# Kernel optimization log

Hardware: AMD Instinct MI355X
Metric: run time of the kernel (lower is better)

## Reference

```python
import jax, jax.numpy as jnp
import numpy as np

EPS = 1e-5
GROUPS = 32


def setup_inputs() -> dict:
    key = jax.random.key(0)
    ks = jax.random.split(key, 12)
    b, c, h, w = 8, 256, 64, 64
    s = 1.0 / np.sqrt(c)
    return {
        "x": jax.random.normal(ks[0], (b, c, h, w), jnp.float32),
        "gn_w": jax.random.uniform(ks[1], (c,), jnp.float32, 0.5, 1.5),
        "gn_b": jax.random.normal(ks[2], (c,), jnp.float32) * 0.1,
        "wq": jax.random.normal(ks[3], (c, c), jnp.float32) * s,
        "bq": jax.random.normal(ks[4], (c,), jnp.float32) * 0.02,
        "wk": jax.random.normal(ks[5], (c, c), jnp.float32) * s,
        "bk": jax.random.normal(ks[6], (c,), jnp.float32) * 0.02,
        "wv": jax.random.normal(ks[7], (c, c), jnp.float32) * s,
        "bv": jax.random.normal(ks[8], (c,), jnp.float32) * 0.02,
        "wp": jax.random.normal(ks[9], (c, c), jnp.float32) * s,
        "bp": jax.random.normal(ks[10], (c,), jnp.float32) * 0.02,
        "gamma": jax.random.normal(ks[11], (1,), jnp.float32),
    }


def _group_norm(x, weight, bias):
    b, c, h, w = x.shape
    g = min(c, GROUPS)
    xg = x.reshape(b, g, c // g, h * w)
    mean = xg.mean(axis=(2, 3), keepdims=True)
    var = jnp.var(xg, axis=(2, 3), keepdims=True)
    xn = (xg - mean) * jax.lax.rsqrt(var + EPS)
    xn = xn.reshape(b, c, h, w)
    return xn * weight[None, :, None, None] + bias[None, :, None, None]


def reference(x, gn_w, gn_b, wq, bq, wk, bk, wv, bv, wp, bp, gamma):
    b, c, h, w = x.shape
    x_dash = _group_norm(x, gn_w, gn_b)           # (b,c,h,w)
    xf = x_dash.reshape(b, c, h * w)              # (b,c,n)
    # 1x1 convs == per-pixel linear maps over channels
    q = jnp.einsum('oc,bcn->bon', wq, xf) + bq[None, :, None]
    k = jnp.einsum('oc,bcn->bon', wk, xf) + bk[None, :, None]
    v = jnp.einsum('oc,bcn->bon', wv, xf) + bv[None, :, None]
    # attn[b,i,j] = <q[:,i], k[:,j]> / sqrt(c)
    attn = jnp.einsum('bci,bcj->bij', q, k) / jnp.sqrt(jnp.asarray(c, x.dtype))
    attn = jax.nn.softmax(attn, axis=-1)
    # out[b,c,i] = sum_j v[b,c,j] * attn[b,i,j]
    out = jnp.einsum('bcj,bij->bci', v, attn)
    out = jnp.einsum('oc,bcn->bon', wp, out) + bp[None, :, None]
    out = out.reshape(b, c, h, w)
    return x + gamma[0] * out
```

## Files before the change

kernel.cpp:

```cpp
#include <hip/hip_runtime.h>
#include <cstdint>
#include <cstddef>


#define NB   8
#define NC   256
#define NPIX 4096
#define CPG  8

typedef __attribute__((ext_vector_type(8))) short bf16x8;
typedef __attribute__((ext_vector_type(4))) short s16x4;
typedef __attribute__((ext_vector_type(8))) short s16x8;
typedef __attribute__((ext_vector_type(4))) float f32x4;

__device__ __forceinline__ short f2bf(float f) {
  union { float f; uint32_t u; } v; v.f = f;
  return (short)((v.u + 0x7fffu + ((v.u >> 16) & 1u)) >> 16);
}

__device__ __forceinline__ uint32_t cvtpk_bf(float a, float b) {
  uint32_t r;
  asm("v_cvt_pk_bf16_f32 %0, %1, %2" : "=v"(r) : "v"(a), "v"(b));
  return r;
}

__device__ __forceinline__ f32x4 mfma16(bf16x8 a, bf16x8 b, f32x4 c) {
  return __builtin_amdgcn_mfma_f32_16x16x32_bf16(a, b, c, 0, 0, 0);
}

__device__ __forceinline__ void gload_lds16(const short* g, short* l) {
  __builtin_amdgcn_global_load_lds(
      (const __attribute__((address_space(1))) void*)g,
      (__attribute__((address_space(3))) void*)l, 16, 0, 0);
}

__global__ __launch_bounds__(256) void wconv4(
    const float* __restrict__ w0, const float* __restrict__ w1,
    const float* __restrict__ w2, const float* __restrict__ w3,
    short* __restrict__ o0, short* __restrict__ o1,
    short* __restrict__ o2, short* __restrict__ o3) {
  int m = blockIdx.x >> 6;
  const float* w = (m == 0) ? w0 : (m == 1) ? w1 : (m == 2) ? w2 : w3;
  short* o = (m == 0) ? o0 : (m == 1) ? o1 : (m == 2) ? o2 : o3;
  int i = ((blockIdx.x & 63) * 256 + threadIdx.x) * 4;
  float4 v = *reinterpret_cast<const float4*>(w + i);
  s16x4 p;
  p[0] = f2bf(v.x); p[1] = f2bf(v.y); p[2] = f2bf(v.z); p[3] = f2bf(v.w);
  *reinterpret_cast<s16x4*>(o + i) = p;
}

__global__ __launch_bounds__(1024) void gnorm(const float* __restrict__ x,
                                              const float* __restrict__ gw,
                                              const float* __restrict__ gb,
                                              short* __restrict__ xdt) {
  int b = blockIdx.x >> 5;
  int g = blockIdx.x & 31;
  const float* xp = x + ((size_t)b * NC + (size_t)g * CPG) * NPIX;
  int t = threadIdx.x;

  float s = 0.f, ss = 0.f;
  const float4* xp4 = reinterpret_cast<const float4*>(xp);
  for (int i = t; i < (CPG * NPIX) / 4; i += 1024) {
    float4 v = xp4[i];
    s  += v.x + v.y + v.z + v.w;
    ss += v.x * v.x + v.y * v.y + v.z * v.z + v.w * v.w;
  }
  for (int m = 32; m; m >>= 1) { s += __shfl_xor(s, m); ss += __shfl_xor(ss, m); }
  __shared__ float red[34];
  int wid = t >> 6;
  if ((t & 63) == 0) { red[wid] = s; red[16 + wid] = ss; }
  __syncthreads();
  if (t == 0) {
    float a = 0.f, b2 = 0.f;
    for (int i = 0; i < 16; ++i) { a += red[i]; b2 += red[16 + i]; }
    float mean = a * (1.f / 32768.f);
    float var  = b2 * (1.f / 32768.f) - mean * mean;
    red[32] = mean;
    red[33] = rsqrtf(var + 1e-5f);
  }
  __syncthreads();
  float mean = red[32], rstd = red[33];

  float wv2[CPG], bv2[CPG];
  for (int cc = 0; cc < CPG; ++cc) {
    float wgt = gw[g * CPG + cc] * rstd;
    wv2[cc] = wgt;
    bv2[cc] = gb[g * CPG + cc] - mean * wgt;
  }
  for (int pix = t; pix < NPIX; pix += 1024) {
    s16x8 pk;
    for (int cc = 0; cc < CPG; ++cc)
      pk[cc] = f2bf(fmaf(xp[cc * NPIX + pix], wv2[cc], bv2[cc]));
    *reinterpret_cast<s16x8*>(&xdt[((size_t)b * NPIX + pix) * NC + g * CPG]) = pk;
  }
}

__global__ __launch_bounds__(256) void qkv_gemm(
    const short* __restrict__ wq_bf, const short* __restrict__ wk_bf,
    const short* __restrict__ wv_bf,
    const float* __restrict__ bq, const float* __restrict__ bk,
    const float* __restrict__ bv,
    const short* __restrict__ xdt,
    short* __restrict__ qt, short* __restrict__ kt, short* __restrict__ vv) {
  int nt = blockIdx.x, b = blockIdx.y;

  __shared__ short xtile[64 * 256];
  __shared__ float bias_lds[3][256];
  int t = threadIdx.x;
  const short* xg = xdt + ((size_t)b * NPIX + nt * 64) * NC;
  for (int it = 0; it < 8; ++it) {
    int id = t + it * 256, row = id >> 5, part = id & 31;
    *reinterpret_cast<uint4*>(&xtile[row * 256 + (part ^ (row & 7)) * 8]) =
        *reinterpret_cast<const uint4*>(&xg[(size_t)row * 256 + part * 8]);
  }
  bias_lds[0][t] = bq[t];
  bias_lds[1][t] = bk[t];
  bias_lds[2][t] = bv[t];
  __syncthreads();

  int w = t >> 6, lane = t & 63, g = lane >> 4, lr = lane & 15;
  const short* Ws[3] = {wq_bf, wk_bf, wv_bf};

  for (int mi = 0; mi < 3; ++mi) {
    const short* W = Ws[mi];
    f32x4 acc[4][4];
    f32x4 zz = {0.f, 0.f, 0.f, 0.f};
    for (int i = 0; i < 4; ++i) for (int j = 0; j < 4; ++j) acc[i][j] = zz;

    for (int c0 = 0; c0 < 256; c0 += 32) {
      bf16x8 af[4], bfr[4];
      for (int mf = 0; mf < 4; ++mf)
        af[mf] = *reinterpret_cast<const bf16x8*>(
            &W[(size_t)(w * 64 + mf * 16 + lr) * 256 + c0 + g * 8]);
      for (int nf = 0; nf < 4; ++nf) {
        int row = nf * 16 + lr;
        bfr[nf] = *reinterpret_cast<const bf16x8*>(
            &xtile[row * 256 + (((c0 >> 3) + g) ^ (row & 7)) * 8]);
      }
      for (int mf = 0; mf < 4; ++mf)
        for (int nf = 0; nf < 4; ++nf)
          acc[mf][nf] = mfma16(af[mf], bfr[nf], acc[mf][nf]);
    }

    if (mi < 2) {
      short* outp = (mi == 0) ? qt : kt;
      for (int mf = 0; mf < 4; ++mf)
        for (int nf = 0; nf < 4; ++nf) {
          int ob = w * 64 + mf * 16 + g * 4;
          int n  = nt * 64 + nf * 16 + lr;
          s16x4 pk;
          for (int r = 0; r < 4; ++r)
            pk[r] = f2bf(acc[mf][nf][r] + bias_lds[mi][ob + r]);
          *reinterpret_cast<s16x4*>(&outp[((size_t)b * NPIX + n) * NC + ob]) = pk;
        }
    } else {
      for (int mf = 0; mf < 4; ++mf)
        for (int nf = 0; nf < 4; ++nf) {
          int ob = w * 64 + mf * 16 + g * 4;
          int n  = nt * 64 + nf * 16 + lr;
          for (int r = 0; r < 4; ++r)
            vv[((size_t)b * NC + ob + r) * NPIX + n] =
                f2bf(acc[mf][nf][r] + bias_lds[2][ob + r]);
        }
    }
  }
}

__global__ __launch_bounds__(256, 2) void attn(
    const short* __restrict__ qt, const short* __restrict__ kt,
    const short* __restrict__ vv, short* __restrict__ ot) {
  int b = blockIdx.x, itile = blockIdx.y;
  __shared__ short ktile[64 * 256];
  __shared__ short Pb[2][64 * 64];
  __shared__ float alpha_lds[2][64];
  __shared__ float exch[2][64];

  int t = threadIdx.x, w = t >> 6, lane = t & 63, g = lane >> 4, lr = lane & 15;
  int kk = w >> 1, qq = w & 1;
  int i0 = itile * 64;

  const short* ktg = kt + (size_t)b * NPIX * NC;

  for (int it = 0; it < 8; ++it) {
    int id = it * 256 + t, row = id >> 5, ch = id & 31;
    gload_lds16(ktg + row * 256 + (ch ^ (row & 7)) * 8, &ktile[id * 8]);
  }
  const short* kgp = ktg + 16384;

  bf16x8 qf[2][8];
  for (int qi = 0; qi < 2; ++qi) {
    const short* qrow =
        qt + ((size_t)b * NPIX + i0 + 32 * qq + 16 * qi + lr) * NC;
    for (int ks = 0; ks < 8; ++ks)
      qf[qi][ks] = *reinterpret_cast<const bf16x8*>(&qrow[ks * 32 + g * 8]);
  }

  const short* vbase =
      vv + (size_t)b * NC * NPIX + (size_t)(w * 64 + lr) * NPIX + g * 8;

  int row0 = 32 * kk + lr, row1 = row0 + 16;
  int eidx[2], pwo[2][2];
  for (int qi = 0; qi < 2; ++qi) {
    int q_loc = 32 * qq + 16 * qi + lr;
    eidx[qi] = q_loc;
    for (int mt = 0; mt < 2; ++mt)
      pwo[qi][mt] = q_loc * 64 +
                    (((4 * kk + 2 * mt + (g >> 1)) ^ (q_loc & 7)) * 8) +
                    (g & 1) * 4;
  }
  int pr[4][2];
  for (int nf = 0; nf < 4; ++nf)
    for (int ks2 = 0; ks2 < 2; ++ks2) {
      int qc = nf * 16 + lr;
      pr[nf][ks2] = qc * 64 + (((ks2 * 4 + g) ^ (qc & 7)) * 8);
    }

  f32x4 zz = {0.f, 0.f, 0.f, 0.f};
  f32x4 oacc[4][4];
  for (int i = 0; i < 4; ++i) for (int j = 0; j < 4; ++j) oacc[i][j] = zz;
  bf16x8 va0[4], va1[4];
  float m_[2] = {-1e30f, -1e30f}, l_p[2] = {0.f, 0.f};

  const float sc = 0.0625f, L2E = 1.44269504f;
  const float SCL = sc * L2E;

  for (int jt = 0; jt < 64; ++jt) {
    int cur = jt & 1, prv = cur ^ 1;

    asm volatile("s_waitcnt vmcnt(0) lgkmcnt(0)" ::: "memory");
    __builtin_amdgcn_s_barrier();
    asm volatile("" ::: "memory");

    if (jt > 0) {
      float av[4];
#pragma unroll
      for (int nf = 0; nf < 4; ++nf) av[nf] = alpha_lds[prv][nf * 16 + lr];
      if (__any((av[0] != 1.f) | (av[1] != 1.f) | (av[2] != 1.f) | (av[3] != 1.f))) {
#pragma unroll
        for (int mf = 0; mf < 4; ++mf)
#pragma unroll
          for (int nf = 0; nf < 4; ++nf) oacc[mf][nf] *= av[nf];
      }
      __builtin_amdgcn_s_setprio(1);
      bf16x8 pb[4];
#pragma unroll
      for (int nf = 0; nf < 4; ++nf)
        pb[nf] = *reinterpret_cast<const bf16x8*>(&Pb[prv][pr[nf][0]]);
#pragma unroll
      for (int mf = 0; mf < 4; ++mf)
#pragma unroll
        for (int nf = 0; nf < 4; ++nf)
          oacc[mf][nf] = mfma16(va0[mf], pb[nf], oacc[mf][nf]);
      __builtin_amdgcn_s_setprio(0);
      const short* vp = vbase + (size_t)(jt - 1) * 64 + 32;
#pragma unroll
      for (int mf = 0; mf < 4; ++mf)
        va1[mf] = *reinterpret_cast<const bf16x8*>(vp + (size_t)mf * (16 * NPIX));
    }

    f32x4 s[2][2];
    s[0][0] = zz; s[0][1] = zz; s[1][0] = zz; s[1][1] = zz;
    __builtin_amdgcn_s_setprio(1);
#pragma unroll
    for (int ks = 0; ks < 8; ++ks) {
      bf16x8 kf0 = *reinterpret_cast<const bf16x8*>(
          &ktile[row0 * 256 + (((ks * 4) + g) ^ (row0 & 7)) * 8]);
      bf16x8 kf1 = *reinterpret_cast<const bf16x8*>(
          &ktile[row1 * 256 + (((ks * 4) + g) ^ (row1 & 7)) * 8]);
      s[0][0] = mfma16(kf0, qf[0][ks], s[0][0]);
      s[0][1] = mfma16(kf0, qf[1][ks], s[0][1]);
      s[1][0] = mfma16(kf1, qf[0][ks], s[1][0]);
      s[1][1] = mfma16(kf1, qf[1][ks], s[1][1]);
    }
    __builtin_amdgcn_s_setprio(0);

    float mx[2];
#pragma unroll
    for (int qi = 0; qi < 2; ++qi) {
      float m0 = fmaxf(fmaxf(s[0][qi][0], s[0][qi][1]),
                       fmaxf(s[0][qi][2], s[0][qi][3]));
      float m1 = fmaxf(fmaxf(s[1][qi][0], s[1][qi][1]),
                       fmaxf(s[1][qi][2], s[1][qi][3]));
      float m = fmaxf(m0, m1);
      m = fmaxf(m, __shfl_xor(m, 16));
      m = fmaxf(m, __shfl_xor(m, 32));
      mx[qi] = m;
    }
    if (lane < 16) {
      exch[kk][32 * qq + lr]      = mx[0];
      exch[kk][32 * qq + 16 + lr] = mx[1];
    }

    asm volatile("s_waitcnt lgkmcnt(0)" ::: "memory");
    __builtin_amdgcn_s_barrier();
    asm volatile("" ::: "memory");

    for (int it = 0; it < 8; ++it) {
      int id = it * 256 + t, row = id >> 5, ch = id & 31;
      gload_lds16(kgp + row * 256 + (ch ^ (row & 7)) * 8, &ktile[id * 8]);
    }
    kgp += 16384;

    if (jt > 0) {
      asm volatile("s_waitcnt vmcnt(8)" ::: "memory");
      __builtin_amdgcn_s_setprio(1);
      bf16x8 pb[4];
#pragma unroll
      for (int nf = 0; nf < 4; ++nf)
        pb[nf] = *reinterpret_cast<const bf16x8*>(&Pb[prv][pr[nf][1]]);
#pragma unroll
      for (int mf = 0; mf < 4; ++mf)
#pragma unroll
        for (int nf = 0; nf < 4; ++nf)
          oacc[mf][nf] = mfma16(va1[mf], pb[nf], oacc[mf][nf]);
      __builtin_amdgcn_s_setprio(0);
    }

    {
      const short* vp = vbase + (size_t)jt * 64;
#pragma unroll
      for (int mf = 0; mf < 4; ++mf)
        va0[mf] = *reinterpret_cast<const bf16x8*>(vp + (size_t)mf * (16 * NPIX));
    }

#pragma unroll
    for (int qi = 0; qi < 2; ++qi) {
      float pm = fmaxf(mx[qi], exch[kk ^ 1][eidx[qi]]) * sc;
      float mn = (pm - m_[qi] <= 8.f) ? m_[qi] : pm;
      float alpha = exp2f((m_[qi] - mn) * L2E);
      float mnl = mn * L2E;
      float ps = 0.f;
#pragma unroll
      for (int mt = 0; mt < 2; ++mt) {
        float p0 = exp2f(fmaf(s[mt][qi][0], SCL, -mnl));
        float p1 = exp2f(fmaf(s[mt][qi][1], SCL, -mnl));
        float p2 = exp2f(fmaf(s[mt][qi][2], SCL, -mnl));
        float p3 = exp2f(fmaf(s[mt][qi][3], SCL, -mnl));
        ps += (p0 + p1) + (p2 + p3);
        uint2 pk;
        pk.x = cvtpk_bf(p0, p1);
        pk.y = cvtpk_bf(p2, p3);
        *reinterpret_cast<uint2*>(&Pb[cur][pwo[qi][mt]]) = pk;
      }
      l_p[qi] = l_p[qi] * alpha + ps;
      m_[qi] = mn;
      if (kk == 0 && lane < 16) alpha_lds[cur][eidx[qi]] = alpha;
    }
  }

  {
    const short* vp = vbase + (size_t)63 * 64 + 32;
#pragma unroll
    for (int mf = 0; mf < 4; ++mf)
      va1[mf] = *reinterpret_cast<const bf16x8*>(vp + (size_t)mf * (16 * NPIX));
  }
  asm volatile("s_waitcnt vmcnt(0) lgkmcnt(0)" ::: "memory");
  __builtin_amdgcn_s_barrier();
  asm volatile("" ::: "memory");
  {
    float av[4];
#pragma unroll
    for (int nf = 0; nf < 4; ++nf) av[nf] = alpha_lds[1][nf * 16 + lr];
    if (__any((av[0] != 1.f) | (av[1] != 1.f) | (av[2] != 1.f) | (av[3] != 1.f))) {
      for (int mf = 0; mf < 4; ++mf)
        for (int nf = 0; nf < 4; ++nf) oacc[mf][nf] *= av[nf];
    }
    bf16x8 pb[4];
#pragma unroll
    for (int nf = 0; nf < 4; ++nf)
      pb[nf] = *reinterpret_cast<const bf16x8*>(&Pb[1][pr[nf][0]]);
    for (int mf = 0; mf < 4; ++mf)
      for (int nf = 0; nf < 4; ++nf)
        oacc[mf][nf] = mfma16(va0[mf], pb[nf], oacc[mf][nf]);
#pragma unroll
    for (int nf = 0; nf < 4; ++nf)
      pb[nf] = *reinterpret_cast<const bf16x8*>(&Pb[1][pr[nf][1]]);
    for (int mf = 0; mf < 4; ++mf)
      for (int nf = 0; nf < 4; ++nf)
        oacc[mf][nf] = mfma16(va1[mf], pb[nf], oacc[mf][nf]);
  }

#pragma unroll
  for (int qi = 0; qi < 2; ++qi) {
    float v = l_p[qi];
    v += __shfl_xor(v, 16);
    v += __shfl_xor(v, 32);
    l_p[qi] = v;
  }
  if (lane < 16) {
    exch[kk][32 * qq + lr]      = l_p[0];
    exch[kk][32 * qq + 16 + lr] = l_p[1];
  }
  __syncthreads();

  for (int nf = 0; nf < 4; ++nf) {
    int q = nf * 16 + lr;
    float inv = 1.f / (exch[0][q] + exch[1][q]);
    int i = i0 + q;
    for (int mf = 0; mf < 4; ++mf) {
      int cb = w * 64 + mf * 16 + g * 4;
      s16x4 pk;
      for (int r = 0; r < 4; ++r) pk[r] = f2bf(oacc[mf][nf][r] * inv);
      *reinterpret_cast<s16x4*>(&ot[((size_t)b * NPIX + i) * NC + cb]) = pk;
    }
  }
}

__global__ __launch_bounds__(256) void proj_res(
    const short* __restrict__ wp_bf, const float* __restrict__ bp,
    const short* __restrict__ ot, const float* __restrict__ x,
    const float* __restrict__ gamma, float* __restrict__ out) {
  int nt = blockIdx.x, b = blockIdx.y;
  __shared__ short otile[64 * 256];
  __shared__ float bias_lds[256];
  int t = threadIdx.x;
  const short* og = ot + ((size_t)b * NPIX + nt * 64) * NC;
  for (int itx = 0; itx < 8; ++itx) {
    int id = t + itx * 256, row = id >> 5, part = id & 31;
    *reinterpret_cast<uint4*>(&otile[row * 256 + (part ^ (row & 7)) * 8]) =
        *reinterpret_cast<const uint4*>(&og[(size_t)row * 256 + part * 8]);
  }
  bias_lds[t] = bp[t];
  __syncthreads();

  int w = t >> 6, lane = t & 63, g = lane >> 4, lr = lane & 15;
  f32x4 acc[4][4];
  f32x4 zz = {0.f, 0.f, 0.f, 0.f};
  for (int i = 0; i < 4; ++i) for (int j = 0; j < 4; ++j) acc[i][j] = zz;

  for (int c0 = 0; c0 < 256; c0 += 32) {
    bf16x8 af[4], bfr[4];
    for (int mf = 0; mf < 4; ++mf)
      af[mf] = *reinterpret_cast<const bf16x8*>(
          &wp_bf[(size_t)(w * 64 + mf * 16 + lr) * 256 + c0 + g * 8]);
    for (int nf = 0; nf < 4; ++nf) {
      int row = nf * 16 + lr;
      bfr[nf] = *reinterpret_cast<const bf16x8*>(
          &otile[row * 256 + (((c0 >> 3) + g) ^ (row & 7)) * 8]);
    }
    for (int mf = 0; mf < 4; ++mf)
      for (int nf = 0; nf < 4; ++nf)
        acc[mf][nf] = mfma16(af[mf], bfr[nf], acc[mf][nf]);
  }

  float gm = gamma[0];
  for (int mf = 0; mf < 4; ++mf)
    for (int nf = 0; nf < 4; ++nf) {
      int ob = w * 64 + mf * 16 + g * 4;
      int n  = nt * 64 + nf * 16 + lr;
      for (int r = 0; r < 4; ++r) {
        size_t idx = ((size_t)b * NC + ob + r) * NPIX + n;
        out[idx] = x[idx] + gm * (acc[mf][nf][r] + bias_lds[ob + r]);
      }
    }
}

extern "C" void kernel_launch(void* const* d_in, const int* in_sizes, int n_in,
                              void* d_out, int out_size, void* d_ws, size_t ws_size,
                              hipStream_t stream) {
  (void)in_sizes; (void)n_in; (void)out_size; (void)ws_size;
  const float* x     = (const float*)d_in[0];
  const float* gn_w  = (const float*)d_in[1];
  const float* gn_b  = (const float*)d_in[2];
  const float* wq    = (const float*)d_in[3];
  const float* bq    = (const float*)d_in[4];
  const float* wk    = (const float*)d_in[5];
  const float* bk    = (const float*)d_in[6];
  const float* wv    = (const float*)d_in[7];
  const float* bv    = (const float*)d_in[8];
  const float* wp    = (const float*)d_in[9];
  const float* bp    = (const float*)d_in[10];
  const float* gamma = (const float*)d_in[11];
  float* out = (float*)d_out;

  char* ws = (char*)d_ws;
  const size_t WSZ = 131072;
  const size_t TSZ = (size_t)NB * NPIX * NC * 2;
  short* wq_bf = (short*)(ws);
  short* wk_bf = (short*)(ws + WSZ);
  short* wv_bf = (short*)(ws + 2 * WSZ);
  short* wp_bf = (short*)(ws + 3 * WSZ);
  short* xdt   = (short*)(ws + 4 * WSZ);
  short* qt    = (short*)(ws + 4 * WSZ + TSZ);
  short* kt    = (short*)(ws + 4 * WSZ + 2 * TSZ);
  short* vv    = (short*)(ws + 4 * WSZ + 3 * TSZ);
  short* ot    = xdt;

  wconv4<<<256, 256, 0, stream>>>(wq, wk, wv, wp, wq_bf, wk_bf, wv_bf, wp_bf);

  gnorm<<<256, 1024, 0, stream>>>(x, gn_w, gn_b, xdt);

  qkv_gemm<<<dim3(64, 8), 256, 0, stream>>>(wq_bf, wk_bf, wv_bf, bq, bk, bv,
                                            xdt, qt, kt, vv);

  attn<<<dim3(8, 64), 256, 0, stream>>>(qt, kt, vv, ot);

  proj_res<<<dim3(64, 8), 256, 0, stream>>>(wp_bf, bp, ot, x, gamma, out);
}
```

Baseline: 284.2 us.

## Split attention over key halves with a merge kernel (flash-decoding style)

Splits the key dimension of the attention kernel into two halves via a third grid dimension, so twice as many blocks run. Each half writes unnormalized bf16 partial outputs plus its running max and sum, and a new merge kernel rescales and combines them. It also raises the launch-bounds occupancy hint from 2 to 3 and issues the V load earlier with an adjusted waitcnt. The cost is extra partial-output traffic, one more kernel launch, and bf16 rounding of the unnormalized partials. The original single-pass path is kept as a fallback when the workspace is too small.

```diff
diff --git a/kernel.cpp b/kernel.cpp
--- a/kernel.cpp
+++ b/kernel.cpp
@@ -16,6 +16,12 @@
 __device__ __forceinline__ short f2bf(float f) {
   union { float f; uint32_t u; } v; v.f = f;
   return (short)((v.u + 0x7fffu + ((v.u >> 16) & 1u)) >> 16);
+}
+
+__device__ __forceinline__ float bf2f(short s) {
+  union { uint32_t u; float f; } v;
+  v.u = ((uint32_t)(unsigned short)s) << 16;
+  return v.f;
 }
 
 __device__ __forceinline__ uint32_t cvtpk_bf(float a, float b) {
@@ -166,10 +172,12 @@
   }
 }
 
-__global__ __launch_bounds__(256, 2) void attn(
+__global__ __launch_bounds__(256, 3) void attn(
     const short* __restrict__ qt, const short* __restrict__ kt,
-    const short* __restrict__ vv, short* __restrict__ ot) {
-  int b = blockIdx.x, itile = blockIdx.y;
+    const short* __restrict__ vv, short* __restrict__ outp,
+    float2* __restrict__ lm, int njt, int final_write) {
+  int b = blockIdx.x, itile = blockIdx.y, kh = blockIdx.z;
+  int jt0 = kh * njt;
   __shared__ short ktile[64 * 256];
   __shared__ short Pb[2][64 * 64];
   __shared__ float alpha_lds[2][64];
@@ -183,9 +191,10 @@
 
   for (int it = 0; it < 8; ++it) {
     int id = it * 256 + t, row = id >> 5, ch = id & 31;
-    gload_lds16(ktg + row * 256 + (ch ^ (row & 7)) * 8, &ktile[id * 8]);
-  }
-  const short* kgp = ktg + 16384;
+    gload_lds16(ktg + (size_t)jt0 * 16384 + row * 256 + (ch ^ (row & 7)) * 8,
+                &ktile[id * 8]);
+  }
+  const short* kgp = ktg + (size_t)(jt0 + 1) * 16384;
 
   bf16x8 qf[2][8];
   for (int qi = 0; qi < 2; ++qi) {
@@ -224,14 +233,15 @@
   const float sc = 0.0625f, L2E = 1.44269504f;
   const float SCL = sc * L2E;
 
-  for (int jt = 0; jt < 64; ++jt) {
-    int cur = jt & 1, prv = cur ^ 1;
+  for (int j = 0; j < njt; ++j) {
+    int jt = jt0 + j;
+    int cur = j & 1, prv = cur ^ 1;
 
     asm volatile("s_waitcnt vmcnt(0) lgkmcnt(0)" ::: "memory");
     __builtin_amdgcn_s_barrier();
     asm volatile("" ::: "memory");
 
-    if (jt > 0) {
+    if (j > 0) {
       float av[4];
 #pragma unroll
       for (int nf = 0; nf < 4; ++nf) av[nf] = alpha_lds[prv][nf * 16 + lr];
@@ -301,8 +311,15 @@
     }
     kgp += 16384;
 
-    if (jt > 0) {
-      asm volatile("s_waitcnt vmcnt(8)" ::: "memory");
+    {
+      const short* vp = vbase + (size_t)jt * 64;
+#pragma unroll
+      for (int mf = 0; mf < 4; ++mf)
+        va0[mf] = *reinterpret_cast<const bf16x8*>(vp + (size_t)mf * (16 * NPIX));
+    }
+
+    if (j > 0) {
+      asm volatile("s_waitcnt vmcnt(12)" ::: "memory");
       __builtin_amdgcn_s_setprio(1);
       bf16x8 pb[4];
 #pragma unroll
@@ -314,13 +331,6 @@
         for (int nf = 0; nf < 4; ++nf)
           oacc[mf][nf] = mfma16(va1[mf], pb[nf], oacc[mf][nf]);
       __builtin_amdgcn_s_setprio(0);
-    }
-
-    {
-      const short* vp = vbase + (size_t)jt * 64;
-#pragma unroll
-      for (int mf = 0; mf < 4; ++mf)
-        va0[mf] = *reinterpret_cast<const bf16x8*>(vp + (size_t)mf * (16 * NPIX));
     }
 
 #pragma unroll
@@ -349,7 +359,7 @@
   }
 
   {
-    const short* vp = vbase + (size_t)63 * 64 + 32;
+    const short* vp = vbase + (size_t)(jt0 + njt - 1) * 64 + 32;
 #pragma unroll
     for (int mf = 0; mf < 4; ++mf)
       va1[mf] = *reinterpret_cast<const bf16x8*>(vp + (size_t)mf * (16 * NPIX));
@@ -393,17 +403,49 @@
   }
   __syncthreads();
 
+  short* okh = outp + (size_t)kh * NB * NPIX * NC;
   for (int nf = 0; nf < 4; ++nf) {
     int q = nf * 16 + lr;
-    float inv = 1.f / (exch[0][q] + exch[1][q]);
+    float inv = final_write ? 1.f / (exch[0][q] + exch[1][q]) : 1.f;
     int i = i0 + q;
     for (int mf = 0; mf < 4; ++mf) {
       int cb = w * 64 + mf * 16 + g * 4;
       s16x4 pk;
       for (int r = 0; r < 4; ++r) pk[r] = f2bf(oacc[mf][nf][r] * inv);
-      *reinterpret_cast<s16x4*>(&ot[((size_t)b * NPIX + i) * NC + cb]) = pk;
-    }
-  }
+      *reinterpret_cast<s16x4*>(&okh[((size_t)b * NPIX + i) * NC + cb]) = pk;
+    }
+  }
+  if (!final_write && w < 2 && lane < 16) {
+    float2* lmk = lm + (size_t)kh * NB * NPIX + (size_t)b * NPIX + i0;
+#pragma unroll
+    for (int qi = 0; qi < 2; ++qi) {
+      int q = 32 * w + 16 * qi + lane;
+      float2 v2;
+      v2.x = m_[qi];
+      v2.y = exch[0][q] + exch[1][q];
+      lmk[q] = v2;
+    }
+  }
+}
+
+__global__ __launch_bounds__(256) void attn_merge(
+    const short* __restrict__ o0, const short* __restrict__ o1,
+    const float2* __restrict__ lm, short* __restrict__ ot) {
+  int idx = (blockIdx.x * 256 + threadIdx.x) * 8;
+  int row = idx >> 8;
+  const float L2E = 1.44269504f;
+  float2 lm0 = lm[row], lm1 = lm[NB * NPIX + row];
+  float M = fmaxf(lm0.x, lm1.x);
+  float f0 = exp2f((lm0.x - M) * L2E), f1 = exp2f((lm1.x - M) * L2E);
+  float inv = 1.f / (f0 * lm0.y + f1 * lm1.y);
+  f0 *= inv; f1 *= inv;
+  s16x8 a = *reinterpret_cast<const s16x8*>(o0 + idx);
+  s16x8 c = *reinterpret_cast<const s16x8*>(o1 + idx);
+  s16x8 o;
+#pragma unroll
+  for (int e = 0; e < 8; ++e)
+    o[e] = f2bf(f0 * bf2f(a[e]) + f1 * bf2f(c[e]));
+  *reinterpret_cast<s16x8*>(ot + idx) = o;
 }
 
 __global__ __launch_bounds__(256) void proj_res(
@@ -458,7 +500,7 @@
 extern "C" void kernel_launch(void* const* d_in, const int* in_sizes, int n_in,
                               void* d_out, int out_size, void* d_ws, size_t ws_size,
                               hipStream_t stream) {
-  (void)in_sizes; (void)n_in; (void)out_size; (void)ws_size;
+  (void)in_sizes; (void)n_in; (void)out_size;
   const float* x     = (const float*)d_in[0];
   const float* gn_w  = (const float*)d_in[1];
   const float* gn_b  = (const float*)d_in[2];
@@ -485,6 +527,9 @@
   short* kt    = (short*)(ws + 4 * WSZ + 2 * TSZ);
   short* vv    = (short*)(ws + 4 * WSZ + 3 * TSZ);
   short* ot    = xdt;
+  short*  opart = (short*)(ws + 4 * WSZ + 4 * TSZ);
+  float2* lmb   = (float2*)(ws + 4 * WSZ + 6 * TSZ);
+  const size_t NEED = 4 * WSZ + 6 * TSZ + (size_t)2 * NB * NPIX * sizeof(float2);
 
   wconv4<<<256, 256, 0, stream>>>(wq, wk, wv, wp, wq_bf, wk_bf, wv_bf, wp_bf);
 
@@ -493,7 +538,13 @@
   qkv_gemm<<<dim3(64, 8), 256, 0, stream>>>(wq_bf, wk_bf, wv_bf, bq, bk, bv,
                                             xdt, qt, kt, vv);
 
-  attn<<<dim3(8, 64), 256, 0, stream>>>(qt, kt, vv, ot);
+  if (ws_size >= NEED) {
+    attn<<<dim3(8, 64, 2), 256, 0, stream>>>(qt, kt, vv, opart, lmb, 32, 0);
+    attn_merge<<<4096, 256, 0, stream>>>(opart, opart + (size_t)NB * NPIX * NC,
+                                         lmb, ot);
+  } else {
+    attn<<<dim3(8, 64, 1), 256, 0, stream>>>(qt, kt, vv, ot, lmb, 64, 1);
+  }
 
   proj_res<<<dim3(64, 8), 256, 0, stream>>>(wp_bf, bp, ot, x, gamma, out);
 }
```

Result: slower. 736.4 us (+159.2%).
